# Optimization experiments

Measured on AMD Instinct MI355X. Metric: run time of the kernel, lower is better.

## Reference

```python
import jax, jax.numpy as jnp
import numpy as np

COMMITMENT_COST = 0.25


def setup_inputs() -> dict:
    key = jax.random.key(0)
    k1, k2 = jax.random.split(key)
    B, S, D, K = 16, 4096, 256, 4096
    inputs = jax.random.normal(k1, (B, S, D), dtype=jnp.float32)
    # codebook ~ embedding.weight (init scale irrelevant for correctness baseline)
    codebook = jax.random.normal(k2, (K, D), dtype=jnp.float32)
    return {"inputs": inputs, "codebook": codebook}


def reference(inputs, codebook):
    B, S, D = inputs.shape
    flat = inputs.reshape(-1, D)  # (N, D)
    distances = (
        jnp.sum(flat * flat, axis=1, keepdims=True)
        + jnp.sum(codebook * codebook, axis=1)
        - 2.0 * jnp.matmul(flat, codebook.T)
    )
    encoding_indices = jnp.argmin(distances, axis=1)  # (N,)
    quantized = codebook[encoding_indices].reshape(inputs.shape)  # gather
    # commitment loss: beta * mse(inputs, sg(quantized))
    diff = inputs - jax.lax.stop_gradient(quantized)
    commitment_loss = COMMITMENT_COST * jnp.mean(diff * diff)
    # straight-through estimator
    quantized_st = inputs + jax.lax.stop_gradient(quantized - inputs)
    return quantized_st, commitment_loss, encoding_indices
```

## Files before the change

kernel.cpp:

```cpp
#include <hip/hip_runtime.h>
#include <stdint.h>

typedef _Float16 half8 __attribute__((ext_vector_type(8)));
typedef float f32x4 __attribute__((ext_vector_type(4)));

#define DDIM 256
#define KCODES 4096
#define BM 128
#define BN 128
#define DELTA 0.10f
#define FLT_BIG 3.4e38f

#define GLOAD_LDS(gsrc, ldst)                                                        \
    __builtin_amdgcn_global_load_lds(                                                \
        (const __attribute__((address_space(1))) void*)(const void*)(gsrc),          \
        (__attribute__((address_space(3))) void*)(void*)(ldst), 16, 0, 0)

__global__ void cvt_h_kernel(const float* __restrict__ src, half8* __restrict__ dst) {
    int gid = blockIdx.x * 256 + threadIdx.x;
    int s = gid & 31;
    long row = gid >> 5;
    const float* p = src + row * DDIM + s * 8;
    const float4 f0 = ((const float4*)p)[0];
    const float4 f1 = ((const float4*)p)[1];
    half8 h;
    h[0] = (_Float16)f0.x; h[1] = (_Float16)f0.y;
    h[2] = (_Float16)f0.z; h[3] = (_Float16)f0.w;
    h[4] = (_Float16)f1.x; h[5] = (_Float16)f1.y;
    h[6] = (_Float16)f1.z; h[7] = (_Float16)f1.w;
    dst[gid] = h;
}

__global__ void enorm_kernel(const float* __restrict__ cb, float* __restrict__ en, int K) {
    int gid = blockIdx.x * blockDim.x + threadIdx.x;
    int code = gid >> 6;
    int lane = threadIdx.x & 63;
    if (code >= K) return;
    const float4 v = *reinterpret_cast<const float4*>(&cb[(size_t)code * DDIM + lane * 4]);
    float s = v.x * v.x + v.y * v.y + v.z * v.z + v.w * v.w;
    #pragma unroll
    for (int off = 32; off > 0; off >>= 1) s += __shfl_xor(s, off, 64);
    if (lane == 0) en[code] = s;
}

__global__ __launch_bounds__(256, 2)
void vq_mfma_kernel(const half8* x16, const half8* __restrict__ cb16,
                    const float* __restrict__ en, int* __restrict__ bidx,
                    int* __restrict__ list, int* __restrict__ counter) {
    __shared__ __align__(16) half8 Abuf[2][BM * 8];
    __shared__ __align__(16) half8 Bbuf[2][BN * 8];
    __shared__ float red_d[2][BM];
    __shared__ float red_d2[2][BM];
    __shared__ int   red_i[2][BM];

    const int tid = threadIdx.x;
    const int lane = tid & 63;
    const int w = tid >> 6;
    const int wr = w >> 1, wc = w & 1;
    const int l15 = lane & 15, l4 = lane >> 4;
    const int brow = blockIdx.x * BM;

    const int lrow = lane >> 3;
    const int swz = (lane & 7) ^ lrow;
    const half8* pA0 = x16 + (size_t)(brow + (w     ) * 8 + lrow) * 32 + swz;
    const half8* pA1 = x16 + (size_t)(brow + (w +  4) * 8 + lrow) * 32 + swz;
    const half8* pA2 = x16 + (size_t)(brow + (w +  8) * 8 + lrow) * 32 + swz;
    const half8* pA3 = x16 + (size_t)(brow + (w + 12) * 8 + lrow) * 32 + swz;
    const half8* pB0 = cb16 + (size_t)((w     ) * 8 + lrow) * 32 + swz;
    const half8* pB1 = cb16 + (size_t)((w +  4) * 8 + lrow) * 32 + swz;
    const half8* pB2 = cb16 + (size_t)((w +  8) * 8 + lrow) * 32 + swz;
    const half8* pB3 = cb16 + (size_t)((w + 12) * 8 + lrow) * 32 + swz;

#define STAGE(b_) do {                                      \
        GLOAD_LDS(pA0, &Abuf[b_][(w     ) * 64]);           \
        GLOAD_LDS(pA1, &Abuf[b_][(w +  4) * 64]);           \
        GLOAD_LDS(pA2, &Abuf[b_][(w +  8) * 64]);           \
        GLOAD_LDS(pA3, &Abuf[b_][(w + 12) * 64]);           \
        GLOAD_LDS(pB0, &Bbuf[b_][(w     ) * 64]);           \
        GLOAD_LDS(pB1, &Bbuf[b_][(w +  4) * 64]);           \
        GLOAD_LDS(pB2, &Bbuf[b_][(w +  8) * 64]);           \
        GLOAD_LDS(pB3, &Bbuf[b_][(w + 12) * 64]);           \
    } while (0)

#define ADVA(dA_, dB_) do {                                 \
        pA0 += dA_; pA1 += dA_; pA2 += dA_; pA3 += dA_;     \
        pB0 += dB_; pB1 += dB_; pB2 += dB_; pB3 += dB_;     \
    } while (0)

    const int sw7 = l15 & 7;
    const int s0 = l4 ^ sw7;
    const _Float16* A0 = (const _Float16*)Abuf;
    const _Float16* B0 = A0 + 16384;
    const _Float16* aH0 = A0 + (wr * 64 + l15) * 64 + s0 * 8;
    const _Float16* aH1 = A0 + (wr * 64 + l15) * 64 + (s0 ^ 4) * 8;
    const _Float16* bH0 = B0 + (wc * 64 + l15) * 64 + s0 * 8;
    const _Float16* bH1 = B0 + (wc * 64 + l15) * 64 + (s0 ^ 4) * 8;

    STAGE(0); ADVA(8, 8);

    float bestv[4], best2v[4];
    int bidv[4];
    #pragma unroll
    for (int i = 0; i < 4; ++i) { bestv[i] = FLT_BIG; best2v[i] = FLT_BIG; bidv[i] = 0; }

    const int code_sub = wc * 64 + l4 * 4;
    f32x4 acc[4][4];

    for (int it = 0; it < 32; ++it) {
        #pragma unroll
        for (int m = 0; m < 4; ++m)
            #pragma unroll
            for (int n = 0; n < 4; ++n) acc[m][n] = (f32x4){0.f, 0.f, 0.f, 0.f};

        #pragma unroll
        for (int k = 0; k < 4; ++k) {
            __syncthreads();
            if (k != 3) {
                STAGE((k + 1) & 1);
                if (k == 2) ADVA(-24, 4072);
                else        ADVA(8, 8);
            } else if (it != 31) {
                STAGE(0);
                ADVA(8, 8);
            }
            __builtin_amdgcn_sched_barrier(0);

            const int o = (k & 1) ? 8192 : 0;
            half8 a0[4], a1[4], b0[4], b1[4];
            #pragma unroll
            for (int i = 0; i < 4; ++i) {
                a0[i] = *(const half8*)(aH0 + o + i * 1024);
                a1[i] = *(const half8*)(aH1 + o + i * 1024);
                b0[i] = *(const half8*)(bH0 + o + i * 1024);
                b1[i] = *(const half8*)(bH1 + o + i * 1024);
            }
            __builtin_amdgcn_s_setprio(1);
            #pragma unroll
            for (int m = 0; m < 4; ++m)
                #pragma unroll
                for (int n = 0; n < 4; ++n) {
                    acc[m][n] = __builtin_amdgcn_mfma_f32_16x16x32_f16(b0[m], a0[n], acc[m][n], 0, 0, 0);
                    acc[m][n] = __builtin_amdgcn_mfma_f32_16x16x32_f16(b1[m], a1[n], acc[m][n], 0, 0, 0);
                }
            __builtin_amdgcn_s_setprio(0);
        }

        const int c0 = it * BN;
        #pragma unroll
        for (int m = 0; m < 4; ++m) {
            const float4 e4 = *(const float4*)(en + c0 + wc * 64 + m * 16 + l4 * 4);
            #pragma unroll
            for (int r = 0; r < 4; ++r) {
                int code = c0 + code_sub + m * 16 + r;
                float e = (r == 0) ? e4.x : (r == 1) ? e4.y : (r == 2) ? e4.z : e4.w;
                #pragma unroll
                for (int n = 0; n < 4; ++n) {
                    float dist = fmaf(-2.f, acc[m][n][r], e);
                    if (dist < bestv[n]) { best2v[n] = bestv[n]; bestv[n] = dist; bidv[n] = code; }
                    else if (dist < best2v[n]) best2v[n] = dist;
                }
            }
        }
    }
#undef STAGE
#undef ADVA

    #pragma unroll
    for (int n = 0; n < 4; ++n) {
        float d = bestv[n], d2 = best2v[n];
        int ix = bidv[n];
        #pragma unroll
        for (int off = 16; off < 64; off <<= 1) {
            float od = __shfl_xor(d, off, 64);
            float od2 = __shfl_xor(d2, off, 64);
            int oi = __shfl_xor(ix, off, 64);
            if (od < d || (od == d && oi < ix)) { d2 = fminf(d, od2); d = od; ix = oi; }
            else d2 = fminf(d2, od);
        }
        if (l4 == 0) {
            int row = wr * 64 + n * 16 + l15;
            red_d[wc][row] = d;
            red_d2[wc][row] = d2;
            red_i[wc][row] = ix;
        }
    }
    __syncthreads();

    if (tid < BM) {
        float d = red_d[0][tid], d2 = red_d2[0][tid];
        int ix = red_i[0][tid];
        float od = red_d[1][tid], od2 = red_d2[1][tid];
        int oi = red_i[1][tid];
        if (od < d || (od == d && oi < ix)) { d2 = fminf(d, od2); d = od; ix = oi; }
        else d2 = fminf(d2, od);
        bidx[brow + tid] = ix;
        if (d2 - d < DELTA) {
            int pos = atomicAdd(counter, 1);
            list[pos] = brow + tid;
        }
    }
}

__global__ __launch_bounds__(256)
void rescan_kernel(const float* __restrict__ x, const float* __restrict__ cb,
                   const float* __restrict__ en, const int* __restrict__ list,
                   const int* __restrict__ counter, int* __restrict__ bidx) {
    __shared__ __align__(16) float4 xrow4[64];
    __shared__ float wd[4];
    __shared__ int wi[4];
    const int tid = threadIdx.x;
    const int w = tid >> 6;
    const int lane = tid & 63;
    const int cnt = *counter;

    for (int it = blockIdx.x; it < cnt; it += gridDim.x) {
        const int row = list[it];
        __syncthreads();
        if (tid < 64) xrow4[tid] = ((const float4*)&x[(size_t)row * DDIM])[tid];
        __syncthreads();
        const float4 xv = xrow4[lane];
        float bd = FLT_BIG;
        int bi = 0;
        for (int i = 0; i < KCODES / 4; ++i) {
            int code = i * 4 + w;
            const float4 c4 = ((const float4*)&cb[(size_t)code * DDIM])[lane];
            float s = xv.x * c4.x + xv.y * c4.y + xv.z * c4.z + xv.w * c4.w;
            #pragma unroll
            for (int off = 1; off < 64; off <<= 1) s += __shfl_xor(s, off, 64);
            float dist = fmaf(-2.f, s, en[code]);
            if (dist < bd) { bd = dist; bi = code; }
        }
        if (lane == 0) { wd[w] = bd; wi[w] = bi; }
        __syncthreads();
        if (tid == 0) {
            float d = wd[0]; int ix = wi[0];
            #pragma unroll
            for (int q = 1; q < 4; ++q) {
                if (wd[q] < d || (wd[q] == d && wi[q] < ix)) { d = wd[q]; ix = wi[q]; }
            }
            bidx[row] = ix;
        }
    }
}

__global__ __launch_bounds__(256)
void gather_kernel(const float* __restrict__ x, const float* __restrict__ cb,
                   const int* __restrict__ bidx, float* __restrict__ out,
                   float* __restrict__ loss_accum, int N) {
    __shared__ float wsum[4];
    __shared__ int bloc[64];
    const int tid = threadIdx.x;
    const int brow = blockIdx.x * 64;
    const size_t ND = (size_t)N * DDIM;
    if (tid < 64) {
        int ix = bidx[brow + tid];
        bloc[tid] = ix;
        out[ND + 1 + brow + tid] = (float)ix;
    }
    __syncthreads();
    float lsum = 0.f;
    #pragma unroll
    for (int pp = 0; pp < 16; ++pp) {
        int i = tid + pp * 256;
        int row = i >> 6;
        int c4 = (i & 63) << 2;
        int code = bloc[row];
        const float4 q = *reinterpret_cast<const float4*>(&cb[(size_t)code * DDIM + c4]);
        const float4 xv = *reinterpret_cast<const float4*>(&x[(size_t)(brow + row) * DDIM + c4]);
        float d0 = xv.x - q.x, d1 = xv.y - q.y, d2 = xv.z - q.z, d3 = xv.w - q.w;
        lsum += d0 * d0 + d1 * d1 + d2 * d2 + d3 * d3;
        *reinterpret_cast<float4*>(&out[(size_t)(brow + row) * DDIM + c4]) = q;
    }
    #pragma unroll
    for (int off = 32; off > 0; off >>= 1) lsum += __shfl_xor(lsum, off, 64);
    if ((tid & 63) == 0) wsum[tid >> 6] = lsum;
    __syncthreads();
    if (tid == 0) {
        float tot = wsum[0] + wsum[1] + wsum[2] + wsum[3];
        atomicAdd(loss_accum, tot * (0.25f / (float)ND));
    }
}

__global__ void loss_fin_kernel(const float* __restrict__ loss_accum,
                                float* __restrict__ out, size_t off) {
    if (blockIdx.x == 0 && threadIdx.x == 0) out[off] = *loss_accum;
}

extern "C" void kernel_launch(void* const* d_in, const int* in_sizes, int n_in,
                              void* d_out, int out_size, void* d_ws, size_t ws_size,
                              hipStream_t stream) {
    const float* x = (const float*)d_in[0];
    const float* cb = (const float*)d_in[1];
    const int N = in_sizes[0] / DDIM;
    const int K = in_sizes[1] / DDIM;
    float* out = (float*)d_out;

    half8* x16 = (half8*)d_out;

    half8* cb16 = (half8*)d_ws;
    char* p = (char*)d_ws + (2 << 20);
    float* en = (float*)p;                  p += (size_t)K * 4;
    int* bidx = (int*)p;                    p += (size_t)N * 4;
    int* list = (int*)p;                    p += (size_t)N * 4;
    int* counter = (int*)p;                 p += 64;
    float* loss_accum = (float*)p;

    hipMemsetAsync(counter, 0, sizeof(int), stream);
    hipMemsetAsync(loss_accum, 0, sizeof(float), stream);
    cvt_h_kernel<<<(N * 32) / 256, 256, 0, stream>>>(x, x16);
    cvt_h_kernel<<<(K * 32) / 256, 256, 0, stream>>>(cb, cb16);
    enorm_kernel<<<(K * 64) / 256, 256, 0, stream>>>(cb, en, K);
    vq_mfma_kernel<<<N / BM, 256, 0, stream>>>(x16, cb16, en, bidx, list, counter);
    rescan_kernel<<<512, 256, 0, stream>>>(x, cb, en, list, counter, bidx);
    gather_kernel<<<N / 64, 256, 0, stream>>>(x, cb, bidx, out, loss_accum, N);
    loss_fin_kernel<<<1, 64, 0, stream>>>(loss_accum, out, (size_t)N * DDIM);
}
```

Measured before the change: 756.0 us.

## Batch rescan over 16 rows per block and fuse codebook convert with norms

The rescan kernel now handles 16 candidate rows per block iteration. Each wave covers a quarter of the codebook, and each lane keeps a 64-element slice of one row in registers, so every codebook load is reused across rows and the shuffle reduction shrinks to two steps. The codebook fp16 conversion and the norm computation are merged into one kernel, removing a launch and a second read of the codebook. DELTA is raised, which flags more rows for the exact rescan: this favours correctness at the cost of extra rescan work.

New measurement: 842.8 us. 11.5% more time.

```diff
diff --git a/kernel.cpp b/kernel.cpp
--- a/kernel.cpp
+++ b/kernel.cpp
@@ -8,7 +8,7 @@
 #define KCODES 4096
 #define BM 128
 #define BN 128
-#define DELTA 0.10f
+#define DELTA 0.12f
 #define FLT_BIG 3.4e38f
 
 #define GLOAD_LDS(gsrc, ldst)                                                        \
@@ -31,16 +31,25 @@
     dst[gid] = h;
 }
 
-__global__ void enorm_kernel(const float* __restrict__ cb, float* __restrict__ en, int K) {
-    int gid = blockIdx.x * blockDim.x + threadIdx.x;
-    int code = gid >> 6;
-    int lane = threadIdx.x & 63;
-    if (code >= K) return;
-    const float4 v = *reinterpret_cast<const float4*>(&cb[(size_t)code * DDIM + lane * 4]);
-    float s = v.x * v.x + v.y * v.y + v.z * v.z + v.w * v.w;
-    #pragma unroll
-    for (int off = 32; off > 0; off >>= 1) s += __shfl_xor(s, off, 64);
-    if (lane == 0) en[code] = s;
+__global__ void cvt_cb_en_kernel(const float* __restrict__ cb, half8* __restrict__ dst,
+                                 float* __restrict__ en) {
+    int gid = blockIdx.x * 256 + threadIdx.x;
+    int s = gid & 31;
+    long row = gid >> 5;
+    const float* p = cb + row * DDIM + s * 8;
+    const float4 f0 = ((const float4*)p)[0];
+    const float4 f1 = ((const float4*)p)[1];
+    half8 h;
+    h[0] = (_Float16)f0.x; h[1] = (_Float16)f0.y;
+    h[2] = (_Float16)f0.z; h[3] = (_Float16)f0.w;
+    h[4] = (_Float16)f1.x; h[5] = (_Float16)f1.y;
+    h[6] = (_Float16)f1.z; h[7] = (_Float16)f1.w;
+    dst[gid] = h;
+    float ss = f0.x * f0.x + f0.y * f0.y + f0.z * f0.z + f0.w * f0.w
+             + f1.x * f1.x + f1.y * f1.y + f1.z * f1.z + f1.w * f1.w;
+    #pragma unroll
+    for (int m = 16; m > 0; m >>= 1) ss += __shfl_xor(ss, m, 64);
+    if (s == 0) en[row] = ss;
 }
 
 __global__ __launch_bounds__(256, 2)
@@ -205,40 +214,78 @@
 void rescan_kernel(const float* __restrict__ x, const float* __restrict__ cb,
                    const float* __restrict__ en, const int* __restrict__ list,
                    const int* __restrict__ counter, int* __restrict__ bidx) {
-    __shared__ __align__(16) float4 xrow4[64];
-    __shared__ float wd[4];
-    __shared__ int wi[4];
+    __shared__ float xs[16 * 260];
+    __shared__ int   rloc[16];
+    __shared__ float sd[4][16];
+    __shared__ int   si[4][16];
     const int tid = threadIdx.x;
+    const int lane = tid & 63;
     const int w = tid >> 6;
-    const int lane = tid & 63;
+    const int r = lane & 15;
+    const int q = lane >> 4;
     const int cnt = *counter;
 
-    for (int it = blockIdx.x; it < cnt; it += gridDim.x) {
-        const int row = list[it];
+    for (int base = blockIdx.x * 16; base < cnt; base += gridDim.x * 16) {
         __syncthreads();
-        if (tid < 64) xrow4[tid] = ((const float4*)&x[(size_t)row * DDIM])[tid];
+        if (tid < 16) {
+            int idx = base + tid;
+            rloc[tid] = list[idx < cnt ? idx : cnt - 1];
+        }
         __syncthreads();
-        const float4 xv = xrow4[lane];
+        {
+            int rr = tid >> 4, c0 = tid & 15;
+            const float4* src = (const float4*)&x[(size_t)rloc[rr] * DDIM];
+            float* dstrow = xs + rr * 260;
+            #pragma unroll
+            for (int j = 0; j < 4; ++j)
+                *(float4*)(dstrow + (c0 + j * 16) * 4) = src[c0 + j * 16];
+        }
+        __syncthreads();
+        float4 xr[16];
+        {
+            const float* rowp = xs + r * 260 + q * 64;
+            #pragma unroll
+            for (int j = 0; j < 16; ++j) xr[j] = *(const float4*)(rowp + j * 4);
+        }
         float bd = FLT_BIG;
         int bi = 0;
-        for (int i = 0; i < KCODES / 4; ++i) {
-            int code = i * 4 + w;
-            const float4 c4 = ((const float4*)&cb[(size_t)code * DDIM])[lane];
-            float s = xv.x * c4.x + xv.y * c4.y + xv.z * c4.z + xv.w * c4.w;
-            #pragma unroll
-            for (int off = 1; off < 64; off <<= 1) s += __shfl_xor(s, off, 64);
-            float dist = fmaf(-2.f, s, en[code]);
+        const float4* cbq = (const float4*)cb + ((size_t)w * 1024) * 64 + q * 16;
+        #pragma unroll 2
+        for (int k = 0; k < 1024; ++k) {
+            float p0 = 0.f, p1 = 0.f, p2 = 0.f, p3 = 0.f;
+            #pragma unroll
+            for (int j = 0; j < 4; ++j) {
+                float4 b0 = cbq[j];
+                float4 b1 = cbq[j + 4];
+                float4 b2 = cbq[j + 8];
+                float4 b3 = cbq[j + 12];
+                p0 = fmaf(xr[j].x, b0.x, p0);      p0 = fmaf(xr[j].y, b0.y, p0);
+                p0 = fmaf(xr[j].z, b0.z, p0);      p0 = fmaf(xr[j].w, b0.w, p0);
+                p1 = fmaf(xr[j + 4].x, b1.x, p1);  p1 = fmaf(xr[j + 4].y, b1.y, p1);
+                p1 = fmaf(xr[j + 4].z, b1.z, p1);  p1 = fmaf(xr[j + 4].w, b1.w, p1);
+                p2 = fmaf(xr[j + 8].x, b2.x, p2);  p2 = fmaf(xr[j + 8].y, b2.y, p2);
+                p2 = fmaf(xr[j + 8].z, b2.z, p2);  p2 = fmaf(xr[j + 8].w, b2.w, p2);
+                p3 = fmaf(xr[j + 12].x, b3.x, p3); p3 = fmaf(xr[j + 12].y, b3.y, p3);
+                p3 = fmaf(xr[j + 12].z, b3.z, p3); p3 = fmaf(xr[j + 12].w, b3.w, p3);
+            }
+            float p = (p0 + p1) + (p2 + p3);
+            p += __shfl_xor(p, 16, 64);
+            p += __shfl_xor(p, 32, 64);
+            int code = w * 1024 + k;
+            float dist = fmaf(-2.f, p, en[code]);
             if (dist < bd) { bd = dist; bi = code; }
-        }
-        if (lane == 0) { wd[w] = bd; wi[w] = bi; }
+            cbq += 64;
+        }
+        if (q == 0) { sd[w][r] = bd; si[w][r] = bi; }
         __syncthreads();
-        if (tid == 0) {
-            float d = wd[0]; int ix = wi[0];
-            #pragma unroll
-            for (int q = 1; q < 4; ++q) {
-                if (wd[q] < d || (wd[q] == d && wi[q] < ix)) { d = wd[q]; ix = wi[q]; }
-            }
-            bidx[row] = ix;
+        if (tid < 16) {
+            float d = sd[0][tid]; int ix = si[0][tid];
+            #pragma unroll
+            for (int ww = 1; ww < 4; ++ww) {
+                float od = sd[ww][tid]; int oi = si[ww][tid];
+                if (od < d || (od == d && oi < ix)) { d = od; ix = oi; }
+            }
+            bidx[rloc[tid]] = ix;
         }
     }
 }
@@ -308,8 +355,7 @@
     hipMemsetAsync(counter, 0, sizeof(int), stream);
     hipMemsetAsync(loss_accum, 0, sizeof(float), stream);
     cvt_h_kernel<<<(N * 32) / 256, 256, 0, stream>>>(x, x16);
-    cvt_h_kernel<<<(K * 32) / 256, 256, 0, stream>>>(cb, cb16);
-    enorm_kernel<<<(K * 64) / 256, 256, 0, stream>>>(cb, en, K);
+    cvt_cb_en_kernel<<<(K * 32) / 256, 256, 0, stream>>>(cb, cb16, en);
     vq_mfma_kernel<<<N / BM, 256, 0, stream>>>(x16, cb16, en, bidx, list, counter);
     rescan_kernel<<<512, 256, 0, stream>>>(x, cb, en, list, counter, bidx);
     gather_kernel<<<N / 64, 256, 0, stream>>>(x, cb, bidx, out, loss_accum, N);
```
